# Performance work log

Hardware: AMD Instinct MI355X
Metric: run time of the kernel (lower is better)

The kernel has to match this reference:

```python
import jax, jax.numpy as jnp
import numpy as np

NUM_HEADS = 32
KV_HEADS = 8
HEAD_DIM = 128
HIDDEN = 4096
Q_DIM = NUM_HEADS * HEAD_DIM      # 4096
KV_DIM = KV_HEADS * HEAD_DIM      # 1024
GROUP = NUM_HEADS // KV_HEADS     # 4 (GQA)
ROPE_THETA = 10000.0
LORA_SCALE = 0.5
BP, S = 4, 1024                   # prefill requests x prefill seq len
BD, L = 64, 2048                  # decode requests x cached kv len
R, NA = 16, 8                     # lora rank, num adapters


def _rope(x, pos):
    # x: [..., n_heads, HEAD_DIM]; pos broadcastable over the token dims of x
    half = x.shape[-1] // 2
    inv = 1.0 / (ROPE_THETA ** (jnp.arange(half, dtype=jnp.float32) / half))
    freqs = pos[..., None].astype(jnp.float32) * inv          # pos.shape + (half,)
    cos = jnp.cos(freqs)[..., None, :]                        # insert head axis
    sin = jnp.sin(freqs)[..., None, :]
    x1, x2 = x[..., :half], x[..., half:]
    return jnp.concatenate([x1 * cos - x2 * sin, x2 * cos + x1 * sin], axis=-1)


def _lora(x, A, B, idx):
    # grouped multi-adapter LoRA: per-request adapter selection
    # x: [b, ..., H]; A: [NA, H, R]; B: [NA, R, D]; idx: [b]
    t = jnp.einsum('b...h,bhr->b...r', x, A[idx])
    return LORA_SCALE * jnp.einsum('b...r,brd->b...d', t, B[idx])


def setup_inputs() -> dict:
    key = jax.random.key(0)
    ks = jax.random.split(key, 16)
    T = BP * S + BD
    w = lambda k, shp: (jax.random.normal(k, shp, jnp.float32) * 0.02)
    return {
        'hidden_states': jax.random.normal(ks[0], (T, HIDDEN), jnp.float32),
        'w_qkv': w(ks[1], (HIDDEN, Q_DIM + 2 * KV_DIM)),
        'w_o': w(ks[2], (Q_DIM, HIDDEN)),
        'k_cache': jax.random.normal(ks[3], (BD, L, KV_HEADS, HEAD_DIM), jnp.float32),
        'v_cache': jax.random.normal(ks[4], (BD, L, KV_HEADS, HEAD_DIM), jnp.float32),
        'lora_a_q': w(ks[5], (NA, HIDDEN, R)),
        'lora_b_q': w(ks[6], (NA, R, Q_DIM)),
        'lora_a_k': w(ks[7], (NA, HIDDEN, R)),
        'lora_b_k': w(ks[8], (NA, R, KV_DIM)),
        'lora_a_v': w(ks[9], (NA, HIDDEN, R)),
        'lora_b_v': w(ks[10], (NA, R, KV_DIM)),
        'lora_a_o': w(ks[11], (NA, Q_DIM, R)),
        'lora_b_o': w(ks[12], (NA, R, HIDDEN)),
        'prefill_adapter_idx': jax.random.randint(ks[13], (BP,), 0, NA),
        'decode_adapter_idx': jax.random.randint(ks[14], (BD,), 0, NA),
    }


def reference(hidden_states, w_qkv, w_o, k_cache, v_cache,
              lora_a_q, lora_b_q, lora_a_k, lora_b_k, lora_a_v, lora_b_v,
              lora_a_o, lora_b_o, prefill_adapter_idx, decode_adapter_idx):
    TP = BP * S
    qkv = hidden_states @ w_qkv
    q, k, v = jnp.split(qkv, [Q_DIM, Q_DIM + KV_DIM], axis=1)

    x_p = hidden_states[:TP].reshape(BP, S, HIDDEN)
    x_d = hidden_states[TP:]

    # apply_lora_weight_kvq: per-request adapters on q/k/v
    q_p = q[:TP].reshape(BP, S, Q_DIM) + _lora(x_p, lora_a_q, lora_b_q, prefill_adapter_idx)
    k_p = k[:TP].reshape(BP, S, KV_DIM) + _lora(x_p, lora_a_k, lora_b_k, prefill_adapter_idx)
    v_p = v[:TP].reshape(BP, S, KV_DIM) + _lora(x_p, lora_a_v, lora_b_v, prefill_adapter_idx)
    q_d = q[TP:] + _lora(x_d, lora_a_q, lora_b_q, decode_adapter_idx)
    k_d = k[TP:] + _lora(x_d, lora_a_k, lora_b_k, decode_adapter_idx)
    v_d = v[TP:] + _lora(x_d, lora_a_v, lora_b_v, decode_adapter_idx)

    scale = 1.0 / np.sqrt(HEAD_DIM).astype(np.float32)

    # ---- prefill: causal self-attention with on-the-fly RoPE ----
    q_p = _rope(q_p.reshape(BP, S, NUM_HEADS, HEAD_DIM), jnp.arange(S, dtype=jnp.float32))
    k_p = _rope(k_p.reshape(BP, S, KV_HEADS, HEAD_DIM), jnp.arange(S, dtype=jnp.float32))
    v_p = v_p.reshape(BP, S, KV_HEADS, HEAD_DIM)
    kr = jnp.repeat(k_p, GROUP, axis=2)
    vr = jnp.repeat(v_p, GROUP, axis=2)
    scores = jnp.einsum('bqhd,bkhd->bhqk', q_p, kr) * scale
    causal = jnp.tril(jnp.ones((S, S), bool))
    scores = jnp.where(causal, scores, -jnp.inf)
    attn = jax.nn.softmax(scores, axis=-1)
    out_p = jnp.einsum('bhqk,bkhd->bqhd', attn, vr).reshape(TP, Q_DIM)

    # ---- decode: one new token per request vs paged KV cache ----
    q_d = _rope(q_d.reshape(BD, NUM_HEADS, HEAD_DIM), jnp.asarray(L, jnp.float32))
    k_new = _rope(k_d.reshape(BD, KV_HEADS, HEAD_DIM), jnp.asarray(L, jnp.float32))
    k_hist = _rope(k_cache, jnp.arange(L, dtype=jnp.float32))
    k_all = jnp.concatenate([k_hist, k_new[:, None]], axis=1)   # [BD, L+1, kvh, hd]
    v_all = jnp.concatenate([v_cache, v_d.reshape(BD, 1, KV_HEADS, HEAD_DIM)], axis=1)
    kr2 = jnp.repeat(k_all, GROUP, axis=2)
    vr2 = jnp.repeat(v_all, GROUP, axis=2)
    s2 = jnp.einsum('bhd,bkhd->bhk', q_d, kr2) * scale
    a2 = jax.nn.softmax(s2, axis=-1)
    out_d = jnp.einsum('bhk,bkhd->bhd', a2, vr2).reshape(BD, Q_DIM)

    # ---- o_proj + apply_lora_weight_attn ----
    attn_raw = jnp.concatenate([out_p, out_d], axis=0)
    o = attn_raw @ w_o
    o_p = o[:TP].reshape(BP, S, HIDDEN) + _lora(attn_raw[:TP].reshape(BP, S, Q_DIM), lora_a_o, lora_b_o, prefill_adapter_idx)
    o_d = o[TP:] + _lora(attn_raw[TP:], lora_a_o, lora_b_o, decode_adapter_idx)
    return jnp.concatenate([o_p.reshape(TP, HIDDEN), o_d], axis=0)
```

## Files before the change

### kernel.cpp

```cpp
#include <hip/hip_runtime.h>

#define NUM_HEADS 32
#define KV_HEADS 8
#define HEAD_DIM 128
#define HIDDEN 4096
#define Q_DIM 4096
#define KV_DIM 1024
#define QKV_DIM 6144
#define GROUP 4
#define BP 4
#define S_LEN 1024
#define BD 64
#define L_CTX 2048
#define RANK 16
#define NA 8
#define TP (BP * S_LEN)
#define T_TOT (TP + BD)
#define M_PAD 4224
#define SCALE 0.08838834764831845f
#define LORA_SCALE 0.5f

typedef float fv4 __attribute__((ext_vector_type(4)));
typedef __bf16 bf16x8 __attribute__((ext_vector_type(8)));
typedef unsigned short usv4 __attribute__((ext_vector_type(4)));
typedef unsigned short u16;

__device__ __forceinline__ float b2f(u16 u) {
    unsigned int x = ((unsigned int)u) << 16;
    return __builtin_bit_cast(float, x);
}
__device__ __forceinline__ u16 f2b(float f) {
    unsigned int u = __builtin_bit_cast(unsigned int, f);
    unsigned int r = u + 0x7fffu + ((u >> 16) & 1u);
    return (u16)(r >> 16);
}
__device__ __forceinline__ void gload_lds16(const void* g, void* l) {
    __builtin_amdgcn_global_load_lds((const __attribute__((address_space(1))) void*)g,
                                     (__attribute__((address_space(3))) void*)l, 16, 0, 0);
}

#define OFF_QKV  ((size_t)0)
#define OFF_ATTN OFF_QKV
#define OFF_HB   ((size_t)51904512)
#define OFF_QP   OFF_HB
#define OFF_WOT  OFF_HB
#define OFF_WQT  ((size_t)86507520)
#define OFF_KP   ((size_t)86507520)
#define OFF_VP   ((size_t)94896128)
#define OFF_QD   ((size_t)103284736)
#define OFF_KD   ((size_t)104333312)
#define OFF_VD   ((size_t)104595456)
#define OFF_T    ((size_t)136839168)
#define OFF_TO   ((size_t)137637888)
#define OFF_COS  ((size_t)137904128)
#define OFF_SIN  ((size_t)138428672)

__global__ void rope_tab_kernel(float* ctab, float* stab) {
    int idx = blockIdx.x * 256 + threadIdx.x;
    if (idx >= 2049 * 64) return;
    int pos = idx >> 6, d = idx & 63;
    float inv = 1.0f / powf(10000.0f, (float)d / 64.0f);
    float f = (float)pos * inv;
    ctab[idx] = cosf(f);
    stab[idx] = sinf(f);
}

__global__ void conv_hidden_kernel(const float* __restrict__ x, u16* __restrict__ y) {
    int gid = blockIdx.x * 256 + threadIdx.x;
    if (gid >= M_PAD * (HIDDEN / 8)) return;
    size_t base = (size_t)gid * 8;
    int row = gid >> 9;
    usv4 lo, hi;
    if (row < T_TOT) {
        fv4 a = *(const fv4*)(x + base);
        fv4 b = *(const fv4*)(x + base + 4);
        lo[0] = f2b(a[0]); lo[1] = f2b(a[1]); lo[2] = f2b(a[2]); lo[3] = f2b(a[3]);
        hi[0] = f2b(b[0]); hi[1] = f2b(b[1]); hi[2] = f2b(b[2]); hi[3] = f2b(b[3]);
    } else {
        lo[0] = 0; lo[1] = 0; lo[2] = 0; lo[3] = 0;
        hi[0] = 0; hi[1] = 0; hi[2] = 0; hi[3] = 0;
    }
    *(usv4*)(y + base) = lo;
    *(usv4*)(y + base + 4) = hi;
}

__global__ __launch_bounds__(256) void transpose_f32_bf16_kernel(const float* __restrict__ in,
                                                                 u16* __restrict__ out,
                                                                 int R, int C) {
    __shared__ float tile[64][65];
    int r0 = blockIdx.y * 64, c0 = blockIdx.x * 64;
    int t = threadIdx.x;
    int tr = t >> 4, tc4 = (t & 15) * 4;
#pragma unroll
    for (int it = 0; it < 4; ++it) {
        int r = tr + it * 16;
        fv4 v = *(const fv4*)(in + (size_t)(r0 + r) * C + c0 + tc4);
        tile[r][tc4 + 0] = v[0]; tile[r][tc4 + 1] = v[1];
        tile[r][tc4 + 2] = v[2]; tile[r][tc4 + 3] = v[3];
    }
    __syncthreads();
#pragma unroll
    for (int it = 0; it < 4; ++it) {
        int c = tr + it * 16;
        usv4 st;
        st[0] = f2b(tile[tc4 + 0][c]); st[1] = f2b(tile[tc4 + 1][c]);
        st[2] = f2b(tile[tc4 + 2][c]); st[3] = f2b(tile[tc4 + 3][c]);
        *(usv4*)(out + (size_t)(c0 + c) * R + r0 + tc4) = st;
    }
}

__global__ __launch_bounds__(256) void lora_a_kernel(const float* __restrict__ x,
                              const float* __restrict__ Aq, const float* __restrict__ Ak,
                              const float* __restrict__ Av,
                              const int* __restrict__ pidx, const int* __restrict__ didx,
                              float* __restrict__ T) {
    __shared__ float xs[4][HIDDEN];
    int t0 = blockIdx.x * 4;
    int tid = threadIdx.x;
    for (int j = tid; j < 4096; j += 256) {
        int tok = j >> 10, off = (j & 1023) * 4;
        *(fv4*)&xs[tok][off] = *(const fv4*)(x + (size_t)(t0 + tok) * HIDDEN + off);
    }
    __syncthreads();
    int w = tid >> 6, lane = tid & 63;
    if (w >= 3) return;
    const float* Ab = (w == 0) ? Aq : (w == 1 ? Ak : Av);
    float acc[4][16];
#pragma unroll
    for (int tk = 0; tk < 4; ++tk)
#pragma unroll
        for (int r = 0; r < 16; ++r) acc[tk][r] = 0.f;
#pragma unroll
    for (int tk = 0; tk < 4; ++tk) {
        int t = t0 + tk;
        int a = (t < TP) ? pidx[t >> 10] : didx[t - TP];
        const float* A = Ab + (size_t)a * HIDDEN * RANK;
        for (int i = 0; i < 64; ++i) {
            int hh = i * 64 + lane;
            float xv = xs[tk][hh];
            const float* Ar = A + (size_t)hh * RANK;
            fv4 a0 = *(const fv4*)Ar, a1 = *(const fv4*)(Ar + 4);
            fv4 a2 = *(const fv4*)(Ar + 8), a3 = *(const fv4*)(Ar + 12);
#pragma unroll
            for (int r = 0; r < 4; ++r) {
                acc[tk][r] += xv * a0[r];
                acc[tk][4 + r] += xv * a1[r];
                acc[tk][8 + r] += xv * a2[r];
                acc[tk][12 + r] += xv * a3[r];
            }
        }
    }
#pragma unroll
    for (int tk = 0; tk < 4; ++tk)
#pragma unroll
        for (int r = 0; r < 16; ++r) {
            float v = acc[tk][r];
            v += __shfl_xor(v, 1); v += __shfl_xor(v, 2); v += __shfl_xor(v, 4);
            v += __shfl_xor(v, 8); v += __shfl_xor(v, 16); v += __shfl_xor(v, 32);
            if (lane == r) T[(size_t)(t0 + tk) * 48 + w * 16 + r] = v;
        }
}

template <int OUT_BF16>
__global__ __launch_bounds__(256) void gemm_bt_kernel(const u16* __restrict__ A,
                                                      const u16* __restrict__ BT,
                                                      void* __restrict__ Cp,
                                                      int Mstore, int N, int K) {
    __shared__ __align__(16) u16 As[2][128 * 32];
    __shared__ __align__(16) u16 Bs[2][128 * 32];
    int tid = threadIdx.x;
    int m0 = blockIdx.y * 128, n0 = blockIdx.x * 128;
    int lane = tid & 63, w = tid >> 6, lr = lane & 15, lg = lane >> 4;
    int wr = w >> 1, wc = w & 1;
    int arow = tid >> 2, acol = (tid & 3) * 8;
    const u16* Ab = A + (size_t)(m0 + arow) * K + acol;
    const u16* Bb = BT + (size_t)(n0 + arow) * K + acol;
    fv4 acc[4][4] = {};
    int nt = K / 32;
#define GSTAGE(buf, kk)                                                             \
    {                                                                               \
        char* Ad = (char*)&As[buf][0] + w * 1024;                                   \
        char* Bd = (char*)&Bs[buf][0] + w * 1024;                                   \
        gload_lds16(Ab + (kk), Ad);                                                 \
        gload_lds16(Ab + (size_t)64 * K + (kk), Ad + 4096);                         \
        gload_lds16(Bb + (kk), Bd);                                                 \
        gload_lds16(Bb + (size_t)64 * K + (kk), Bd + 4096);                         \
    }
    GSTAGE(0, 0)
    __syncthreads();
    int cur = 0;
    for (int t = 0; t < nt; ++t) {
        if (t + 1 < nt) GSTAGE(cur ^ 1, (t + 1) * 32)
        bf16x8 af[4], bf[4];
#pragma unroll
        for (int i = 0; i < 4; ++i) {
            af[i] = *(const bf16x8*)&As[cur][(wr * 64 + i * 16 + lr) * 32 + lg * 8];
            bf[i] = *(const bf16x8*)&Bs[cur][(wc * 64 + i * 16 + lr) * 32 + lg * 8];
        }
#pragma unroll
        for (int mi = 0; mi < 4; ++mi)
#pragma unroll
            for (int ni = 0; ni < 4; ++ni)
                acc[mi][ni] = __builtin_amdgcn_mfma_f32_16x16x32_bf16(af[mi], bf[ni], acc[mi][ni], 0, 0, 0);
        __syncthreads();
        cur ^= 1;
    }
#undef GSTAGE
#pragma unroll
    for (int mi = 0; mi < 4; ++mi)
#pragma unroll
        for (int ni = 0; ni < 4; ++ni) {
            int col = n0 + wc * 64 + ni * 16 + lr;
#pragma unroll
            for (int r = 0; r < 4; ++r) {
                int row = m0 + wr * 64 + mi * 16 + lg * 4 + r;
                if (row < Mstore) {
                    if (OUT_BF16)
                        ((u16*)Cp)[(size_t)row * N + col] = f2b(acc[mi][ni][r]);
                    else
                        ((float*)Cp)[(size_t)row * N + col] = acc[mi][ni][r];
                }
            }
        }
}

__global__ __launch_bounds__(256) void lorab_rope_scatter_kernel(
    const u16* __restrict__ qkv, const float* __restrict__ T,
    const float* __restrict__ Bq, const float* __restrict__ Bk, const float* __restrict__ Bv,
    const int* __restrict__ pidx, const int* __restrict__ didx,
    const float* __restrict__ ctab, const float* __restrict__ stab,
    u16* __restrict__ qp, u16* __restrict__ kp, u16* __restrict__ vp,
    float* __restrict__ qd, float* __restrict__ kd, float* __restrict__ vd) {
    int t = blockIdx.x;
    __shared__ float Ts[48];
    if (threadIdx.x < 48) Ts[threadIdx.x] = T[(size_t)t * 48 + threadIdx.x];
    __syncthreads();
    bool pre = t < TP;
    int a = pre ? pidx[t >> 10] : didx[t - TP];
    int pos = pre ? (t & 1023) : L_CTX;
    int b = t >> 10;
    int td = t - TP;
    const u16* qrow = qkv + (size_t)t * QKV_DIM;
    for (int p = threadIdx.x; p < 3072; p += 256) {
        if (p < 2048) {
            int h = p >> 6, d = p & 63;
            int col = h * 128 + d;
            float v1 = b2f(qrow[col]), v2 = b2f(qrow[col + 64]);
            const float* B = Bq + (size_t)a * RANK * Q_DIM;
            float l1 = 0.f, l2 = 0.f;
#pragma unroll
            for (int r = 0; r < 16; ++r) {
                float tv = Ts[r];
                l1 += tv * B[(size_t)r * Q_DIM + col];
                l2 += tv * B[(size_t)r * Q_DIM + col + 64];
            }
            v1 += LORA_SCALE * l1; v2 += LORA_SCALE * l2;
            float c = ctab[pos * 64 + d], s = stab[pos * 64 + d];
            float o1 = v1 * c - v2 * s, o2 = v2 * c + v1 * s;
            if (pre) {
                size_t base = (((size_t)(b * 32 + h)) * 1024 + pos) * 128 + d;
                qp[base] = f2b(o1); qp[base + 64] = f2b(o2);
            } else {
                size_t base = ((size_t)(td * 32 + h)) * 128 + d;
                qd[base] = o1; qd[base + 64] = o2;
            }
        } else if (p < 2560) {
            int pp = p - 2048;
            int h = pp >> 6, d = pp & 63;
            int jc = h * 128 + d;
            int col = Q_DIM + jc;
            float v1 = b2f(qrow[col]), v2 = b2f(qrow[col + 64]);
            const float* B = Bk + (size_t)a * RANK * KV_DIM;
            float l1 = 0.f, l2 = 0.f;
#pragma unroll
            for (int r = 0; r < 16; ++r) {
                float tv = Ts[16 + r];
                l1 += tv * B[(size_t)r * KV_DIM + jc];
                l2 += tv * B[(size_t)r * KV_DIM + jc + 64];
            }
            v1 += LORA_SCALE * l1; v2 += LORA_SCALE * l2;
            float c = ctab[pos * 64 + d], s = stab[pos * 64 + d];
            float o1 = v1 * c - v2 * s, o2 = v2 * c + v1 * s;
            if (pre) {
                size_t base = (((size_t)(b * 8 + h)) * 1024 + pos) * 128 + d;
                kp[base] = f2b(o1); kp[base + 64] = f2b(o2);
            } else {
                size_t base = ((size_t)(td * 8 + h)) * 128 + d;
                kd[base] = o1; kd[base + 64] = o2;
            }
        } else {
            int pp = p - 2560;
            int h = pp >> 6, d = pp & 63;
            int jc = h * 128 + d;
            int col = Q_DIM + KV_DIM + jc;
            float v1 = b2f(qrow[col]), v2 = b2f(qrow[col + 64]);
            const float* B = Bv + (size_t)a * RANK * KV_DIM;
            float l1 = 0.f, l2 = 0.f;
#pragma unroll
            for (int r = 0; r < 16; ++r) {
                float tv = Ts[32 + r];
                l1 += tv * B[(size_t)r * KV_DIM + jc];
                l2 += tv * B[(size_t)r * KV_DIM + jc + 64];
            }
            v1 += LORA_SCALE * l1; v2 += LORA_SCALE * l2;
            if (pre) {
                size_t base = (((size_t)(b * 8 + h)) * 1024 + pos) * 128 + d;
                vp[base] = f2b(v1); vp[base + 64] = f2b(v2);
            } else {
                size_t base = ((size_t)(td * 8 + h)) * 128 + d;
                vd[base] = v1; vd[base + 64] = v2;
            }
        }
    }
}

__global__ __launch_bounds__(256) void prefill_attn_kernel(const u16* __restrict__ qp,
                                                           const u16* __restrict__ kp,
                                                           const u16* __restrict__ vp,
                                                           u16* __restrict__ attn) {
    int bx = blockIdx.x;
    int qt = (bx & 1) ? (31 - (bx >> 1)) : (bx >> 1);
    int kvh = blockIdx.y, b = blockIdx.z;
    int tid = threadIdx.x, w = tid >> 6, lane = tid & 63, lr = lane & 15, lg = lane >> 4;
    int h = kvh * 4 + w;
    const u16* Q = qp + ((size_t)(b * 32 + h)) * 1024 * 128;
    const u16* K = kp + ((size_t)(b * 8 + kvh)) * 1024 * 128;
    const u16* V = vp + ((size_t)(b * 8 + kvh)) * 1024 * 128;
    int qc0 = qt * 32 + lr, qc1 = qt * 32 + 16 + lr;
    bf16x8 qf0[4], qf1[4];
#pragma unroll
    for (int dc = 0; dc < 4; ++dc) {
        qf0[dc] = *(const bf16x8*)(Q + (size_t)qc0 * 128 + dc * 32 + lg * 8);
        qf1[dc] = *(const bf16x8*)(Q + (size_t)qc1 * 128 + dc * 32 + lg * 8);
    }
    fv4 o0[8] = {}, o1[8] = {};
    float m0 = -INFINITY, l0 = 0.f;
    float m1 = -INFINITY, l1 = 0.f;
    int nkb = qt + 1;
    for (int kb = 0; kb < nkb; ++kb) {
        int k0 = kb * 32;
        fv4 s00 = {}, s10 = {}, s01 = {}, s11 = {};
#pragma unroll
        for (int dc = 0; dc < 4; ++dc) {
            bf16x8 kf0 = *(const bf16x8*)(K + (size_t)(k0 + lr) * 128 + dc * 32 + lg * 8);
            bf16x8 kf1 = *(const bf16x8*)(K + (size_t)(k0 + 16 + lr) * 128 + dc * 32 + lg * 8);
            s00 = __builtin_amdgcn_mfma_f32_16x16x32_bf16(kf0, qf0[dc], s00, 0, 0, 0);
            s10 = __builtin_amdgcn_mfma_f32_16x16x32_bf16(kf1, qf0[dc], s10, 0, 0, 0);
            s01 = __builtin_amdgcn_mfma_f32_16x16x32_bf16(kf0, qf1[dc], s01, 0, 0, 0);
            s11 = __builtin_amdgcn_mfma_f32_16x16x32_bf16(kf1, qf1[dc], s11, 0, 0, 0);
        }
        bf16x8 vf[8];
#pragma unroll
        for (int c = 0; c < 8; ++c)
#pragma unroll
            for (int i = 0; i < 4; ++i) {
                vf[c][i] = __builtin_bit_cast(__bf16, V[(size_t)(k0 + lg * 4 + i) * 128 + c * 16 + lr]);
                vf[c][4 + i] = __builtin_bit_cast(__bf16, V[(size_t)(k0 + 16 + lg * 4 + i) * 128 + c * 16 + lr]);
            }
        bf16x8 pf0, pf1;
        {
            float p0[4], p1[4];
            float lm = -INFINITY;
#pragma unroll
            for (int r = 0; r < 4; ++r) {
                float x = s00[r] * SCALE;
                if (k0 + lg * 4 + r > qc0) x = -INFINITY;
                p0[r] = x; lm = fmaxf(lm, x);
                x = s10[r] * SCALE;
                if (k0 + 16 + lg * 4 + r > qc0) x = -INFINITY;
                p1[r] = x; lm = fmaxf(lm, x);
            }
            lm = fmaxf(lm, __shfl_xor(lm, 16));
            lm = fmaxf(lm, __shfl_xor(lm, 32));
            float mn = fmaxf(m0, lm);
            float sc = __expf(m0 - mn);
            float rs = 0.f;
#pragma unroll
            for (int r = 0; r < 4; ++r) {
                p0[r] = __expf(p0[r] - mn);
                p1[r] = __expf(p1[r] - mn);
                rs += p0[r] + p1[r];
            }
            rs += __shfl_xor(rs, 16);
            rs += __shfl_xor(rs, 32);
            l0 = l0 * sc + rs;
            m0 = mn;
#pragma unroll
            for (int c = 0; c < 8; ++c) o0[c] *= sc;
#pragma unroll
            for (int r = 0; r < 4; ++r) {
                pf0[r] = (__bf16)p0[r];
                pf0[4 + r] = (__bf16)p1[r];
            }
        }
        {
            float p0[4], p1[4];
            float lm = -INFINITY;
#pragma unroll
            for (int r = 0; r < 4; ++r) {
                float x = s01[r] * SCALE;
                if (k0 + lg * 4 + r > qc1) x = -INFINITY;
                p0[r] = x; lm = fmaxf(lm, x);
                x = s11[r] * SCALE;
                if (k0 + 16 + lg * 4 + r > qc1) x = -INFINITY;
                p1[r] = x; lm = fmaxf(lm, x);
            }
            lm = fmaxf(lm, __shfl_xor(lm, 16));
            lm = fmaxf(lm, __shfl_xor(lm, 32));
            float mn = fmaxf(m1, lm);
            float sc = __expf(m1 - mn);
            float rs = 0.f;
#pragma unroll
            for (int r = 0; r < 4; ++r) {
                p0[r] = __expf(p0[r] - mn);
                p1[r] = __expf(p1[r] - mn);
                rs += p0[r] + p1[r];
            }
            rs += __shfl_xor(rs, 16);
            rs += __shfl_xor(rs, 32);
            l1 = l1 * sc + rs;
            m1 = mn;
#pragma unroll
            for (int c = 0; c < 8; ++c) o1[c] *= sc;
#pragma unroll
            for (int r = 0; r < 4; ++r) {
                pf1[r] = (__bf16)p0[r];
                pf1[4 + r] = (__bf16)p1[r];
            }
        }
#pragma unroll
        for (int c = 0; c < 8; ++c) {
            o0[c] = __builtin_amdgcn_mfma_f32_16x16x32_bf16(vf[c], pf0, o0[c], 0, 0, 0);
            o1[c] = __builtin_amdgcn_mfma_f32_16x16x32_bf16(vf[c], pf1, o1[c], 0, 0, 0);
        }
    }
    float inv0 = 1.0f / l0, inv1 = 1.0f / l1;
    size_t trow0 = (size_t)(b * 1024 + qc0) * Q_DIM;
    size_t trow1 = (size_t)(b * 1024 + qc1) * Q_DIM;
#pragma unroll
    for (int c = 0; c < 8; ++c)
#pragma unroll
        for (int r = 0; r < 4; ++r) {
            int feat = h * 128 + c * 16 + lg * 4 + r;
            attn[trow0 + feat] = f2b(o0[c][r] * inv0);
            attn[trow1 + feat] = f2b(o1[c][r] * inv1);
        }
}

__global__ __launch_bounds__(512) void decode_attn_kernel(const float* __restrict__ kc,
                                                          const float* __restrict__ vc,
                                                          const float* __restrict__ qd,
                                                          const float* __restrict__ kd,
                                                          const float* __restrict__ vd,
                                                          const float* __restrict__ ctab,
                                                          const float* __restrict__ stab,
                                                          u16* __restrict__ attn) {
    int blk = blockIdx.x;
    int b = blk >> 3, kvh = blk & 7;
    int tid = threadIdx.x, wv = tid >> 6, lane = tid & 63;
    float q1[4], q2[4];
#pragma unroll
    for (int g = 0; g < 4; ++g) {
        size_t qb = ((size_t)(b * 32 + kvh * 4 + g)) * 128;
        q1[g] = qd[qb + lane];
        q2[g] = qd[qb + 64 + lane];
    }
    float m[4], l[4], o1[4], o2[4];
#pragma unroll
    for (int g = 0; g < 4; ++g) { m[g] = -INFINITY; l[g] = 0.f; o1[g] = 0.f; o2[g] = 0.f; }
    for (int key = wv; key <= L_CTX; key += 8) {
        float kr1, kr2, v1, v2;
        if (key < L_CTX) {
            size_t base = (((size_t)b * L_CTX + key) * 8 + kvh) * 128;
            float k1 = kc[base + lane], k2 = kc[base + 64 + lane];
            float c = ctab[key * 64 + lane], s = stab[key * 64 + lane];
            kr1 = k1 * c - k2 * s;
            kr2 = k2 * c + k1 * s;
            v1 = vc[base + lane];
            v2 = vc[base + 64 + lane];
        } else {
            size_t base = ((size_t)(b * 8 + kvh)) * 128;
            kr1 = kd[base + lane]; kr2 = kd[base + 64 + lane];
            v1 = vd[base + lane]; v2 = vd[base + 64 + lane];
        }
#pragma unroll
        for (int g = 0; g < 4; ++g) {
            float part = q1[g] * kr1 + q2[g] * kr2;
#pragma unroll
            for (int off = 32; off; off >>= 1) part += __shfl_xor(part, off);
            float sg = part * SCALE;
            float mn = fmaxf(m[g], sg);
            float sc = __expf(m[g] - mn);
            float p = __expf(sg - mn);
            l[g] = l[g] * sc + p;
            o1[g] = o1[g] * sc + p * v1;
            o2[g] = o2[g] * sc + p * v2;
            m[g] = mn;
        }
    }
    __shared__ float lm[8][4], ll[8][4];
    __shared__ float lo[8][4][128];
#pragma unroll
    for (int g = 0; g < 4; ++g) {
        lo[wv][g][lane] = o1[g];
        lo[wv][g][64 + lane] = o2[g];
    }
    if (lane == 0)
#pragma unroll
        for (int g = 0; g < 4; ++g) { lm[wv][g] = m[g]; ll[wv][g] = l[g]; }
    __syncthreads();
    int g = tid >> 7, d = tid & 127;
    float M = -INFINITY;
#pragma unroll
    for (int wvi = 0; wvi < 8; ++wvi) M = fmaxf(M, lm[wvi][g]);
    float L = 0.f, O = 0.f;
#pragma unroll
    for (int wvi = 0; wvi < 8; ++wvi) {
        float e = __expf(lm[wvi][g] - M);
        L += ll[wvi][g] * e;
        O += lo[wvi][g][d] * e;
    }
    attn[(size_t)(TP + b) * Q_DIM + (kvh * 4 + g) * 128 + d] = f2b(O / L);
}

__global__ __launch_bounds__(64) void lora_o_a_kernel(const u16* __restrict__ attn,
                                const float* __restrict__ Ao,
                                const int* __restrict__ pidx, const int* __restrict__ didx,
                                float* __restrict__ To) {
    __shared__ float xs[4][HIDDEN];
    int t0 = blockIdx.x * 4;
    int lane = threadIdx.x;
    for (int j = lane; j < 4096; j += 64) {
        int tok = j >> 10, off = (j & 1023) * 4;
        usv4 v = *(const usv4*)(attn + (size_t)(t0 + tok) * Q_DIM + off);
        xs[tok][off] = b2f(v[0]); xs[tok][off + 1] = b2f(v[1]);
        xs[tok][off + 2] = b2f(v[2]); xs[tok][off + 3] = b2f(v[3]);
    }
    __syncthreads();
    float acc[4][16];
#pragma unroll
    for (int tk = 0; tk < 4; ++tk)
#pragma unroll
        for (int r = 0; r < 16; ++r) acc[tk][r] = 0.f;
#pragma unroll
    for (int tk = 0; tk < 4; ++tk) {
        int t = t0 + tk;
        int a = (t < TP) ? pidx[t >> 10] : didx[t - TP];
        const float* A = Ao + (size_t)a * Q_DIM * RANK;
        for (int i = 0; i < 64; ++i) {
            int hh = i * 64 + lane;
            float xv = xs[tk][hh];
            const float* Ar = A + (size_t)hh * RANK;
            fv4 a0 = *(const fv4*)Ar, a1 = *(const fv4*)(Ar + 4);
            fv4 a2 = *(const fv4*)(Ar + 8), a3 = *(const fv4*)(Ar + 12);
#pragma unroll
            for (int r = 0; r < 4; ++r) {
                acc[tk][r] += xv * a0[r];
                acc[tk][4 + r] += xv * a1[r];
                acc[tk][8 + r] += xv * a2[r];
                acc[tk][12 + r] += xv * a3[r];
            }
        }
    }
#pragma unroll
    for (int tk = 0; tk < 4; ++tk)
#pragma unroll
        for (int r = 0; r < 16; ++r) {
            float v = acc[tk][r];
            v += __shfl_xor(v, 1); v += __shfl_xor(v, 2); v += __shfl_xor(v, 4);
            v += __shfl_xor(v, 8); v += __shfl_xor(v, 16); v += __shfl_xor(v, 32);
            if (lane == r) To[(size_t)(t0 + tk) * RANK + r] = v;
        }
}

__global__ void final_lora_add_kernel(float* __restrict__ out, const float* __restrict__ To,
                                      const float* __restrict__ Bo,
                                      const int* __restrict__ pidx, const int* __restrict__ didx) {
    int gid = blockIdx.x * 256 + threadIdx.x;
    if (gid >= T_TOT * HIDDEN) return;
    int t = gid >> 12, j = gid & 4095;
    int a = (t < TP) ? pidx[t >> 10] : didx[t - TP];
    const float* B = Bo + (size_t)a * RANK * HIDDEN;
    const float* Tr = To + (size_t)t * RANK;
    float acc = 0.f;
#pragma unroll
    for (int r = 0; r < 16; ++r) acc += Tr[r] * B[(size_t)r * HIDDEN + j];
    out[gid] += LORA_SCALE * acc;
}

extern "C" void kernel_launch(void* const* d_in, const int* in_sizes, int n_in,
                              void* d_out, int out_size, void* d_ws, size_t ws_size,
                              hipStream_t stream) {
    const float* hidden = (const float*)d_in[0];
    const float* w_qkv = (const float*)d_in[1];
    const float* w_o = (const float*)d_in[2];
    const float* k_cache = (const float*)d_in[3];
    const float* v_cache = (const float*)d_in[4];
    const float* Aq = (const float*)d_in[5];
    const float* Bq = (const float*)d_in[6];
    const float* Ak = (const float*)d_in[7];
    const float* Bk = (const float*)d_in[8];
    const float* Av = (const float*)d_in[9];
    const float* Bv = (const float*)d_in[10];
    const float* Ao = (const float*)d_in[11];
    const float* Bo = (const float*)d_in[12];
    const int* pidx = (const int*)d_in[13];
    const int* didx = (const int*)d_in[14];
    float* out = (float*)d_out;

    char* ws = (char*)d_ws;
    u16* qkv = (u16*)(ws + OFF_QKV);
    u16* attn = (u16*)(ws + OFF_ATTN);
    u16* hb = (u16*)(ws + OFF_HB);
    u16* wqT = (u16*)(ws + OFF_WQT);
    u16* woT = (u16*)(ws + OFF_WOT);
    float* T = (float*)(ws + OFF_T);
    u16* qp = (u16*)(ws + OFF_QP);
    u16* kp = (u16*)(ws + OFF_KP);
    u16* vp = (u16*)(ws + OFF_VP);
    float* qd = (float*)(ws + OFF_QD);
    float* kd = (float*)(ws + OFF_KD);
    float* vd = (float*)(ws + OFF_VD);
    float* To = (float*)(ws + OFF_TO);
    float* ctab = (float*)(ws + OFF_COS);
    float* stab = (float*)(ws + OFF_SIN);

    rope_tab_kernel<<<513, 256, 0, stream>>>(ctab, stab);
    conv_hidden_kernel<<<(M_PAD * (HIDDEN / 8) + 255) / 256, 256, 0, stream>>>(hidden, hb);
    transpose_f32_bf16_kernel<<<dim3(QKV_DIM / 64, HIDDEN / 64), 256, 0, stream>>>(w_qkv, wqT, HIDDEN, QKV_DIM);
    lora_a_kernel<<<T_TOT / 4, 256, 0, stream>>>(hidden, Aq, Ak, Av, pidx, didx, T);
    gemm_bt_kernel<1><<<dim3(QKV_DIM / 128, M_PAD / 128), 256, 0, stream>>>(hb, wqT, qkv, M_PAD, QKV_DIM, HIDDEN);
    lorab_rope_scatter_kernel<<<T_TOT, 256, 0, stream>>>(qkv, T, Bq, Bk, Bv, pidx, didx,
                                                         ctab, stab, qp, kp, vp, qd, kd, vd);
    prefill_attn_kernel<<<dim3(32, 8, 4), 256, 0, stream>>>(qp, kp, vp, attn);
    decode_attn_kernel<<<512, 512, 0, stream>>>(k_cache, v_cache, qd, kd, vd, ctab, stab, attn);
    transpose_f32_bf16_kernel<<<dim3(HIDDEN / 64, Q_DIM / 64), 256, 0, stream>>>(w_o, woT, Q_DIM, HIDDEN);
    lora_o_a_kernel<<<T_TOT / 4, 64, 0, stream>>>(attn, Ao, pidx, didx, To);
    gemm_bt_kernel<0><<<dim3(HIDDEN / 128, M_PAD / 128), 256, 0, stream>>>(attn, woT, out, T_TOT, HIDDEN, Q_DIM);
    final_lora_add_kernel<<<(T_TOT * HIDDEN + 255) / 256, 256, 0, stream>>>(out, To, Bo, pidx, didx);
}
```

Measured before the change: 1.664 ms.

## Split decode attention across key ranges with a separate merge kernel

Decode attention now launches four blocks per (request, kv-head), each covering a 512-key slice of the cache and writing partial max, sum and output to a workspace buffer. A new merge kernel combines the partials with log-sum-exp rescaling and writes the bf16 output. This aims to raise parallelism and latency hiding for the memory-bound cache scan, at the cost of an extra launch and a small partial-result round trip.

```diff
diff --git a/kernel.cpp b/kernel.cpp
--- a/kernel.cpp
+++ b/kernel.cpp
@@ -19,6 +19,9 @@
 #define M_PAD 4224
 #define SCALE 0.08838834764831845f
 #define LORA_SCALE 0.5f
+#define NSPLIT 4
+#define SPLIT_LEN 512
+#define DP_STRIDE 520
 
 typedef float fv4 __attribute__((ext_vector_type(4)));
 typedef __bf16 bf16x8 __attribute__((ext_vector_type(8)));
@@ -50,6 +53,7 @@
 #define OFF_QD   ((size_t)103284736)
 #define OFF_KD   ((size_t)104333312)
 #define OFF_VD   ((size_t)104595456)
+#define OFF_DP   ((size_t)104857600)
 #define OFF_T    ((size_t)136839168)
 #define OFF_TO   ((size_t)137637888)
 #define OFF_COS  ((size_t)137904128)
@@ -454,9 +458,11 @@
                                                           const float* __restrict__ vd,
                                                           const float* __restrict__ ctab,
                                                           const float* __restrict__ stab,
-                                                          u16* __restrict__ attn) {
+                                                          float* __restrict__ dp) {
     int blk = blockIdx.x;
-    int b = blk >> 3, kvh = blk & 7;
+    int s = blk & 3;
+    int bk = blk >> 2;
+    int b = bk >> 3, kvh = bk & 7;
     int tid = threadIdx.x, wv = tid >> 6, lane = tid & 63;
     float q1[4], q2[4];
 #pragma unroll
@@ -468,14 +474,17 @@
     float m[4], l[4], o1[4], o2[4];
 #pragma unroll
     for (int g = 0; g < 4; ++g) { m[g] = -INFINITY; l[g] = 0.f; o1[g] = 0.f; o2[g] = 0.f; }
-    for (int key = wv; key <= L_CTX; key += 8) {
+    int kbeg = s * SPLIT_LEN, kend = kbeg + SPLIT_LEN;
+    int klast = (s == NSPLIT - 1 && wv == 0) ? (L_CTX + 8) : kend;
+    for (int key = kbeg + wv; key < klast; key += 8) {
+        if (key > L_CTX) break;
         float kr1, kr2, v1, v2;
         if (key < L_CTX) {
             size_t base = (((size_t)b * L_CTX + key) * 8 + kvh) * 128;
             float k1 = kc[base + lane], k2 = kc[base + 64 + lane];
-            float c = ctab[key * 64 + lane], s = stab[key * 64 + lane];
-            kr1 = k1 * c - k2 * s;
-            kr2 = k2 * c + k1 * s;
+            float c = ctab[key * 64 + lane], ssn = stab[key * 64 + lane];
+            kr1 = k1 * c - k2 * ssn;
+            kr2 = k2 * c + k1 * ssn;
             v1 = vc[base + lane];
             v2 = vc[base + 64 + lane];
         } else {
@@ -519,6 +528,29 @@
         float e = __expf(lm[wvi][g] - M);
         L += ll[wvi][g] * e;
         O += lo[wvi][g][d] * e;
+    }
+    size_t base = ((size_t)(bk * NSPLIT + s)) * DP_STRIDE;
+    dp[base + 8 + g * 128 + d] = O;
+    if (d == 0) { dp[base + g] = M; dp[base + 4 + g] = L; }
+}
+
+__global__ void decode_merge_kernel(const float* __restrict__ dp, u16* __restrict__ attn) {
+    int gid = blockIdx.x * 256 + threadIdx.x;
+    if (gid >= BD * KV_HEADS * 4 * 128) return;
+    int d = gid & 127, g = (gid >> 7) & 3;
+    int kvh = (gid >> 9) & 7, b = gid >> 12;
+    int bk = b * 8 + kvh;
+    float M = -INFINITY;
+#pragma unroll
+    for (int s = 0; s < NSPLIT; ++s)
+        M = fmaxf(M, dp[((size_t)(bk * NSPLIT + s)) * DP_STRIDE + g]);
+    float L = 0.f, O = 0.f;
+#pragma unroll
+    for (int s = 0; s < NSPLIT; ++s) {
+        size_t base = ((size_t)(bk * NSPLIT + s)) * DP_STRIDE;
+        float e = __expf(dp[base + g] - M);
+        L += dp[base + 4 + g] * e;
+        O += dp[base + 8 + g * 128 + d] * e;
     }
     attn[(size_t)(TP + b) * Q_DIM + (kvh * 4 + g) * 128 + d] = f2b(O / L);
 }
@@ -621,6 +653,7 @@
     float* qd = (float*)(ws + OFF_QD);
     float* kd = (float*)(ws + OFF_KD);
     float* vd = (float*)(ws + OFF_VD);
+    float* dp = (float*)(ws + OFF_DP);
     float* To = (float*)(ws + OFF_TO);
     float* ctab = (float*)(ws + OFF_COS);
     float* stab = (float*)(ws + OFF_SIN);
@@ -633,7 +666,8 @@
     lorab_rope_scatter_kernel<<<T_TOT, 256, 0, stream>>>(qkv, T, Bq, Bk, Bv, pidx, didx,
                                                          ctab, stab, qp, kp, vp, qd, kd, vd);
     prefill_attn_kernel<<<dim3(32, 8, 4), 256, 0, stream>>>(qp, kp, vp, attn);
-    decode_attn_kernel<<<512, 512, 0, stream>>>(k_cache, v_cache, qd, kd, vd, ctab, stab, attn);
+    decode_attn_kernel<<<512 * NSPLIT, 512, 0, stream>>>(k_cache, v_cache, qd, kd, vd, ctab, stab, dp);
+    decode_merge_kernel<<<(BD * KV_HEADS * 4 * 128 + 255) / 256, 256, 0, stream>>>(dp, attn);
     transpose_f32_bf16_kernel<<<dim3(HIDDEN / 64, Q_DIM / 64), 256, 0, stream>>>(w_o, woT, Q_DIM, HIDDEN);
     lora_o_a_kernel<<<T_TOT / 4, 64, 0, stream>>>(attn, Ao, pidx, didx, To);
     gemm_bt_kernel<0><<<dim3(HIDDEN / 128, M_PAD / 128), 256, 0, stream>>>(attn, woT, out, T_TOT, HIDDEN, Q_DIM);
```

Result: no change. 1.632 ms (-1.9%).

## Split decode attention across KV chunks with MFMA and add merge kernel

Applied to the files above, without the earlier changes.

Decode attention now runs as flash-decoding. Each wave handles a 128-key chunk and computes QK and PV with bf16 MFMA instructions, in place of scalar shuffles. Per-split max, sum and partial outputs go to a workspace buffer, and a new merge kernel combines them with the new-token contribution. This raises parallelism from 512 blocks to 4096 and removes the per-key shuffle reductions. The cost is an extra launch, a partial-result round trip, bf16 rounding of K, V and Q, and strided V loads.

```diff
diff --git a/kernel.cpp b/kernel.cpp
--- a/kernel.cpp
+++ b/kernel.cpp
@@ -19,6 +19,9 @@
 #define M_PAD 4224
 #define SCALE 0.08838834764831845f
 #define LORA_SCALE 0.5f
+#define DNSPLIT 16
+#define DSPLIT_LEN 128
+#define DP_STRIDE 520
 
 typedef float fv4 __attribute__((ext_vector_type(4)));
 typedef __bf16 bf16x8 __attribute__((ext_vector_type(8)));
@@ -50,6 +53,7 @@
 #define OFF_QD   ((size_t)103284736)
 #define OFF_KD   ((size_t)104333312)
 #define OFF_VD   ((size_t)104595456)
+#define OFF_DP   ((size_t)104857600)
 #define OFF_T    ((size_t)136839168)
 #define OFF_TO   ((size_t)137637888)
 #define OFF_COS  ((size_t)137904128)
@@ -447,80 +451,178 @@
         }
 }
 
-__global__ __launch_bounds__(512) void decode_attn_kernel(const float* __restrict__ kc,
+template <int FIRST_HALF>
+__device__ __forceinline__ bf16x8 krope8(const float* __restrict__ Krow,
+                                         const float* __restrict__ ct,
+                                         const float* __restrict__ st, int d0) {
+    bf16x8 out;
+    if (FIRST_HALF) {
+        fv4 a0 = *(const fv4*)(Krow + d0), a1 = *(const fv4*)(Krow + d0 + 4);
+        fv4 b0 = *(const fv4*)(Krow + d0 + 64), b1 = *(const fv4*)(Krow + d0 + 68);
+        fv4 c0 = *(const fv4*)(ct + d0), c1 = *(const fv4*)(ct + d0 + 4);
+        fv4 s0 = *(const fv4*)(st + d0), s1 = *(const fv4*)(st + d0 + 4);
+#pragma unroll
+        for (int i = 0; i < 4; ++i) {
+            out[i] = (__bf16)(a0[i] * c0[i] - b0[i] * s0[i]);
+            out[4 + i] = (__bf16)(a1[i] * c1[i] - b1[i] * s1[i]);
+        }
+    } else {
+        int dd = d0 - 64;
+        fv4 a0 = *(const fv4*)(Krow + d0), a1 = *(const fv4*)(Krow + d0 + 4);
+        fv4 b0 = *(const fv4*)(Krow + dd), b1 = *(const fv4*)(Krow + dd + 4);
+        fv4 c0 = *(const fv4*)(ct + dd), c1 = *(const fv4*)(ct + dd + 4);
+        fv4 s0 = *(const fv4*)(st + dd), s1 = *(const fv4*)(st + dd + 4);
+#pragma unroll
+        for (int i = 0; i < 4; ++i) {
+            out[i] = (__bf16)(a0[i] * c0[i] + b0[i] * s0[i]);
+            out[4 + i] = (__bf16)(a1[i] * c1[i] + b1[i] * s1[i]);
+        }
+    }
+    return out;
+}
+
+__global__ __launch_bounds__(128) void decode_attn_kernel(const float* __restrict__ kc,
                                                           const float* __restrict__ vc,
                                                           const float* __restrict__ qd,
-                                                          const float* __restrict__ kd,
-                                                          const float* __restrict__ vd,
                                                           const float* __restrict__ ctab,
                                                           const float* __restrict__ stab,
-                                                          u16* __restrict__ attn) {
+                                                          float* __restrict__ dp) {
     int blk = blockIdx.x;
-    int b = blk >> 3, kvh = blk & 7;
-    int tid = threadIdx.x, wv = tid >> 6, lane = tid & 63;
-    float q1[4], q2[4];
-#pragma unroll
-    for (int g = 0; g < 4; ++g) {
-        size_t qb = ((size_t)(b * 32 + kvh * 4 + g)) * 128;
-        q1[g] = qd[qb + lane];
-        q2[g] = qd[qb + 64 + lane];
-    }
-    float m[4], l[4], o1[4], o2[4];
-#pragma unroll
-    for (int g = 0; g < 4; ++g) { m[g] = -INFINITY; l[g] = 0.f; o1[g] = 0.f; o2[g] = 0.f; }
-    for (int key = wv; key <= L_CTX; key += 8) {
-        float kr1, kr2, v1, v2;
-        if (key < L_CTX) {
-            size_t base = (((size_t)b * L_CTX + key) * 8 + kvh) * 128;
-            float k1 = kc[base + lane], k2 = kc[base + 64 + lane];
-            float c = ctab[key * 64 + lane], s = stab[key * 64 + lane];
-            kr1 = k1 * c - k2 * s;
-            kr2 = k2 * c + k1 * s;
-            v1 = vc[base + lane];
-            v2 = vc[base + 64 + lane];
-        } else {
-            size_t base = ((size_t)(b * 8 + kvh)) * 128;
-            kr1 = kd[base + lane]; kr2 = kd[base + 64 + lane];
-            v1 = vd[base + lane]; v2 = vd[base + 64 + lane];
-        }
-#pragma unroll
-        for (int g = 0; g < 4; ++g) {
-            float part = q1[g] * kr1 + q2[g] * kr2;
-#pragma unroll
-            for (int off = 32; off; off >>= 1) part += __shfl_xor(part, off);
-            float sg = part * SCALE;
-            float mn = fmaxf(m[g], sg);
-            float sc = __expf(m[g] - mn);
-            float p = __expf(sg - mn);
-            l[g] = l[g] * sc + p;
-            o1[g] = o1[g] * sc + p * v1;
-            o2[g] = o2[g] * sc + p * v2;
-            m[g] = mn;
-        }
-    }
-    __shared__ float lm[8][4], ll[8][4];
-    __shared__ float lo[8][4][128];
-#pragma unroll
-    for (int g = 0; g < 4; ++g) {
-        lo[wv][g][lane] = o1[g];
-        lo[wv][g][64 + lane] = o2[g];
-    }
-    if (lane == 0)
-#pragma unroll
-        for (int g = 0; g < 4; ++g) { lm[wv][g] = m[g]; ll[wv][g] = l[g]; }
-    __syncthreads();
-    int g = tid >> 7, d = tid & 127;
-    float M = -INFINITY;
-#pragma unroll
-    for (int wvi = 0; wvi < 8; ++wvi) M = fmaxf(M, lm[wvi][g]);
-    float L = 0.f, O = 0.f;
-#pragma unroll
-    for (int wvi = 0; wvi < 8; ++wvi) {
-        float e = __expf(lm[wvi][g] - M);
-        L += ll[wvi][g] * e;
-        O += lo[wvi][g][d] * e;
-    }
-    attn[(size_t)(TP + b) * Q_DIM + (kvh * 4 + g) * 128 + d] = f2b(O / L);
+    int bk = blk >> 3;
+    int b = bk >> 3, kvh = bk & 7;
+    int wv = threadIdx.x >> 6, lane = threadIdx.x & 63;
+    int s = (blk & 7) * 2 + wv;
+    int lr = lane & 15, lg = lane >> 4;
+    const float* Qrow = qd + ((size_t)(b * 32 + kvh * 4 + (lr & 3))) * 128;
+    bf16x8 qf[4];
+#pragma unroll
+    for (int dc = 0; dc < 4; ++dc) {
+        int d0 = dc * 32 + lg * 8;
+        fv4 q0 = *(const fv4*)(Qrow + d0), q1 = *(const fv4*)(Qrow + d0 + 4);
+#pragma unroll
+        for (int i = 0; i < 4; ++i) {
+            qf[dc][i] = (__bf16)q0[i];
+            qf[dc][4 + i] = (__bf16)q1[i];
+        }
+    }
+    fv4 o[8] = {};
+    float m = -INFINITY, l = 0.f;
+    int kbase = s * DSPLIT_LEN;
+    for (int t = 0; t < 4; ++t) {
+        int k0 = kbase + t * 32;
+        int key0 = k0 + lr, key1 = k0 + 16 + lr;
+        const float* K0 = kc + (((size_t)b * L_CTX + key0) * 8 + kvh) * 128;
+        const float* K1 = kc + (((size_t)b * L_CTX + key1) * 8 + kvh) * 128;
+        const float* ct0 = ctab + key0 * 64;
+        const float* st0 = stab + key0 * 64;
+        const float* ct1 = ctab + key1 * 64;
+        const float* st1 = stab + key1 * 64;
+        fv4 s0 = {}, s1 = {};
+#pragma unroll
+        for (int dc = 0; dc < 4; ++dc) {
+            int d0 = dc * 32 + lg * 8;
+            bf16x8 kf0, kf1;
+            if (dc < 2) {
+                kf0 = krope8<1>(K0, ct0, st0, d0);
+                kf1 = krope8<1>(K1, ct1, st1, d0);
+            } else {
+                kf0 = krope8<0>(K0, ct0, st0, d0);
+                kf1 = krope8<0>(K1, ct1, st1, d0);
+            }
+            s0 = __builtin_amdgcn_mfma_f32_16x16x32_bf16(kf0, qf[dc], s0, 0, 0, 0);
+            s1 = __builtin_amdgcn_mfma_f32_16x16x32_bf16(kf1, qf[dc], s1, 0, 0, 0);
+        }
+        const float* Vb = vc + (((size_t)b * L_CTX + k0) * 8 + kvh) * 128;
+        bf16x8 vf[8];
+#pragma unroll
+        for (int c = 0; c < 8; ++c)
+#pragma unroll
+            for (int i = 0; i < 4; ++i) {
+                vf[c][i] = (__bf16)Vb[(size_t)(lg * 4 + i) * 1024 + c * 16 + lr];
+                vf[c][4 + i] = (__bf16)Vb[(size_t)(16 + lg * 4 + i) * 1024 + c * 16 + lr];
+            }
+        float p0[4], p1[4];
+        float lm = -INFINITY;
+#pragma unroll
+        for (int r = 0; r < 4; ++r) {
+            float x = s0[r] * SCALE;
+            p0[r] = x; lm = fmaxf(lm, x);
+            x = s1[r] * SCALE;
+            p1[r] = x; lm = fmaxf(lm, x);
+        }
+        lm = fmaxf(lm, __shfl_xor(lm, 16));
+        lm = fmaxf(lm, __shfl_xor(lm, 32));
+        float mn = fmaxf(m, lm);
+        float sc = __expf(m - mn);
+        float rs = 0.f;
+#pragma unroll
+        for (int r = 0; r < 4; ++r) {
+            p0[r] = __expf(p0[r] - mn);
+            p1[r] = __expf(p1[r] - mn);
+            rs += p0[r] + p1[r];
+        }
+        rs += __shfl_xor(rs, 16);
+        rs += __shfl_xor(rs, 32);
+        l = l * sc + rs;
+        m = mn;
+#pragma unroll
+        for (int c = 0; c < 8; ++c) o[c] *= sc;
+        bf16x8 pf;
+#pragma unroll
+        for (int r = 0; r < 4; ++r) {
+            pf[r] = (__bf16)p0[r];
+            pf[4 + r] = (__bf16)p1[r];
+        }
+#pragma unroll
+        for (int c = 0; c < 8; ++c)
+            o[c] = __builtin_amdgcn_mfma_f32_16x16x32_bf16(vf[c], pf, o[c], 0, 0, 0);
+    }
+    size_t base = ((size_t)(bk * DNSPLIT + s)) * DP_STRIDE;
+    if (lr < 4) {
+#pragma unroll
+        for (int c = 0; c < 8; ++c)
+#pragma unroll
+            for (int r = 0; r < 4; ++r)
+                dp[base + 8 + lr * 128 + c * 16 + lg * 4 + r] = o[c][r];
+        if (lg == 0) { dp[base + lr] = m; dp[base + 4 + lr] = l; }
+    }
+}
+
+__global__ __launch_bounds__(256) void decode_merge_kernel(const float* __restrict__ dp,
+                                                           const float* __restrict__ qd,
+                                                           const float* __restrict__ kd,
+                                                           const float* __restrict__ vd,
+                                                           u16* __restrict__ attn) {
+    int bk = blockIdx.x;
+    int b = bk >> 3, kvh = bk & 7;
+    int g = threadIdx.x >> 6, lane = threadIdx.x & 63;
+    size_t qb = ((size_t)(b * 32 + kvh * 4 + g)) * 128;
+    float q1 = qd[qb + lane], q2 = qd[qb + 64 + lane];
+    size_t kb = ((size_t)(b * 8 + kvh)) * 128;
+    float k1 = kd[kb + lane], k2 = kd[kb + 64 + lane];
+    float v1 = vd[kb + lane], v2 = vd[kb + 64 + lane];
+    float part = q1 * k1 + q2 * k2;
+#pragma unroll
+    for (int off = 32; off; off >>= 1) part += __shfl_xor(part, off);
+    float snew = part * SCALE;
+    float M = snew;
+#pragma unroll
+    for (int s = 0; s < DNSPLIT; ++s)
+        M = fmaxf(M, dp[((size_t)(bk * DNSPLIT + s)) * DP_STRIDE + g]);
+    float L = 0.f, O1 = 0.f, O2 = 0.f;
+#pragma unroll
+    for (int s = 0; s < DNSPLIT; ++s) {
+        size_t base = ((size_t)(bk * DNSPLIT + s)) * DP_STRIDE;
+        float e = __expf(dp[base + g] - M);
+        L += dp[base + 4 + g] * e;
+        O1 += dp[base + 8 + g * 128 + lane] * e;
+        O2 += dp[base + 8 + g * 128 + 64 + lane] * e;
+    }
+    float en = __expf(snew - M);
+    L += en; O1 += en * v1; O2 += en * v2;
+    size_t orow = (size_t)(TP + b) * Q_DIM + (kvh * 4 + g) * 128;
+    attn[orow + lane] = f2b(O1 / L);
+    attn[orow + 64 + lane] = f2b(O2 / L);
 }
 
 __global__ __launch_bounds__(64) void lora_o_a_kernel(const u16* __restrict__ attn,
@@ -621,6 +723,7 @@
     float* qd = (float*)(ws + OFF_QD);
     float* kd = (float*)(ws + OFF_KD);
     float* vd = (float*)(ws + OFF_VD);
+    float* dp = (float*)(ws + OFF_DP);
     float* To = (float*)(ws + OFF_TO);
     float* ctab = (float*)(ws + OFF_COS);
     float* stab = (float*)(ws + OFF_SIN);
@@ -633,7 +736,8 @@
     lorab_rope_scatter_kernel<<<T_TOT, 256, 0, stream>>>(qkv, T, Bq, Bk, Bv, pidx, didx,
                                                          ctab, stab, qp, kp, vp, qd, kd, vd);
     prefill_attn_kernel<<<dim3(32, 8, 4), 256, 0, stream>>>(qp, kp, vp, attn);
-    decode_attn_kernel<<<512, 512, 0, stream>>>(k_cache, v_cache, qd, kd, vd, ctab, stab, attn);
+    decode_attn_kernel<<<4096, 128, 0, stream>>>(k_cache, v_cache, qd, ctab, stab, dp);
+    decode_merge_kernel<<<512, 256, 0, stream>>>(dp, qd, kd, vd, attn);
     transpose_f32_bf16_kernel<<<dim3(HIDDEN / 64, Q_DIM / 64), 256, 0, stream>>>(w_o, woT, Q_DIM, HIDDEN);
     lora_o_a_kernel<<<T_TOT / 4, 64, 0, stream>>>(attn, Ao, pidx, didx, To);
     gemm_bt_kernel<0><<<dim3(HIDDEN / 128, M_PAD / 128), 256, 0, stream>>>(attn, woT, out, T_TOT, HIDDEN, Q_DIM);
```

After: 1.589 ms, median of 2. -4.5%, faster.
